# Kernel tuning notes

Measured on AMD Instinct MI355X. Metric: run time of the kernel, lower is better.

## Reference

```python
import jax, jax.numpy as jnp
import numpy as np

N, IN_DIM, HID, B, C = 131072, 256, 256, 8, 128


def setup_inputs() -> dict:
    key = jax.random.key(0)
    ks = jax.random.split(key, 7)
    s_in, s_h = 1.0 / np.sqrt(IN_DIM), 1.0 / np.sqrt(HID)
    return {
        "x": jax.random.normal(ks[0], (N, IN_DIM), dtype=jnp.float32),
        "W_base": jax.random.normal(ks[1], (IN_DIM, HID), dtype=jnp.float32) * s_in,
        "b_base": jax.random.normal(ks[2], (HID,), dtype=jnp.float32) * 0.01,
        "W_clf": jax.random.normal(ks[3], (B, HID, C), dtype=jnp.float32) * s_h,
        "b_clf": jax.random.normal(ks[4], (B, C), dtype=jnp.float32) * 0.01,
        "W_est": jax.random.normal(ks[5], (B, HID), dtype=jnp.float32) * s_h,
        "b_est": jax.random.normal(ks[6], (B,), dtype=jnp.float32) * 0.01,
    }


def reference(x, W_base, b_base, W_clf, b_clf, W_est, b_est):
    # base trunk: [N, HID]
    base_out = x @ W_base + b_base
    # per-branch estimated loss: [N, B]  (each branch's estimate_loss -> (N,1), viewed as (N,))
    est = base_out @ W_est.T + b_est
    # top-1 routing: per-sample argmin over branches (detached in original)
    branch_ids = jnp.argmin(est, axis=1)  # [N] int
    # all-branch logits [N, B, C]; selecting row branch_ids[n] reproduces the
    # per-branch gather -> forward -> scatter of the original exactly
    logits = jnp.einsum("nh,bhc->nbc", base_out, W_clf) + b_clf
    out = jnp.take_along_axis(logits, branch_ids[:, None, None], axis=1)[:, 0, :]  # [N, C]
    return out
```

## Files before the change

### kernel.cpp

```cpp
#include <hip/hip_runtime.h>


#define NROWS 131072

typedef __bf16 bf16x8 __attribute__((ext_vector_type(8)));
typedef float  f32x4  __attribute__((ext_vector_type(4)));
typedef unsigned short u16x8 __attribute__((ext_vector_type(8)));

__device__ __forceinline__ unsigned short f2bf(float f) {
    unsigned u = __builtin_bit_cast(unsigned, f);
    u += 0x7fffu + ((u >> 16) & 1u);
    return (unsigned short)(u >> 16);
}

__global__ __launch_bounds__(256) void k_prep(const float* __restrict__ Wb,
                                              const float* __restrict__ bb,
                                              const float* __restrict__ Wc,
                                              const float* __restrict__ bc,
                                              const float* __restrict__ We,
                                              const float* __restrict__ be,
                                              double* __restrict__ Wcomb,
                                              double* __restrict__ bcomb,
                                              unsigned short* __restrict__ Wfold,
                                              float* __restrict__ bfold,
                                              int* __restrict__ gzero) {
    __shared__ float clf[32][128];
    __shared__ float wbt[32][16];
    __shared__ double red[256];
    int blk = blockIdx.x, tid = threadIdx.x;

    if (blk < 8) {
        if (blk == 0 && tid < 16) gzero[tid] = 0;
        int b = blk, k = tid;
        const float4* wbr = (const float4*)(Wb + k * 256);
        const float4* wer = (const float4*)(We + b * 256);
        double a0 = 0.0, a1 = 0.0, a2 = 0.0, a3 = 0.0;
#pragma unroll 8
        for (int j = 0; j < 64; ++j) {
            float4 u = wbr[j], w = wer[j];
            a0 += (double)u.x * (double)w.x;
            a1 += (double)u.y * (double)w.y;
            a2 += (double)u.z * (double)w.z;
            a3 += (double)u.w * (double)w.w;
        }
        Wcomb[b * 256 + k] = (a0 + a1) + (a2 + a3);

        red[k] = (double)bb[k] * (double)We[b * 256 + k];
        __syncthreads();
        for (int s = 128; s; s >>= 1) {
            if (k < s) red[k] += red[k + s];
            __syncthreads();
        }
        if (k == 0) bcomb[b] = red[0] + (double)be[b];
        return;
    }

    if (blk < 12) {
        int b = (blk - 8) * 2 + (tid >> 7);
        int c = tid & 127;
        float a = bc[b * 128 + c];
        for (int h = 0; h < 256; ++h)
            a += bb[h] * Wc[(b * 256 + h) * 128 + c];
        bfold[b * 128 + c] = a;
        return;
    }

    int idx0 = blk - 12;
    int kg = idx0 & 15, b = idx0 >> 4;
    int c = tid & 127, kh = tid >> 7;

    float acc[8];
#pragma unroll
    for (int j = 0; j < 8; ++j) acc[j] = 0.f;

    for (int ht = 0; ht < 8; ++ht) {
#pragma unroll
        for (int j = 0; j < 16; ++j) {
            int idx = tid + j * 256;
            int hh = idx >> 7, cc = idx & 127;
            clf[hh][cc] = Wc[(b * 256 + ht * 32 + hh) * 128 + cc];
        }
#pragma unroll
        for (int j = 0; j < 2; ++j) {
            int idx = tid + j * 256;
            int hh = idx & 31, kk = idx >> 5;
            wbt[hh][kk] = Wb[(kg * 16 + kk) * 256 + ht * 32 + hh];
        }
        __syncthreads();
        for (int h = 0; h < 32; ++h) {
            float wc = clf[h][c];
            float4 w0 = *(const float4*)&wbt[h][kh * 8];
            float4 w1 = *(const float4*)&wbt[h][kh * 8 + 4];
            acc[0] += w0.x * wc; acc[1] += w0.y * wc;
            acc[2] += w0.z * wc; acc[3] += w0.w * wc;
            acc[4] += w1.x * wc; acc[5] += w1.y * wc;
            acc[6] += w1.z * wc; acc[7] += w1.w * wc;
        }
        __syncthreads();
    }
    unsigned short o8[8];
#pragma unroll
    for (int j = 0; j < 8; ++j) o8[j] = f2bf(acc[j]);
    u16x8 pk;
#pragma unroll
    for (int j = 0; j < 8; ++j) pk[j] = o8[j];
    int base = (b * 128 + c) * 256 + kg * 16 + kh * 8;
    *(u16x8*)&Wfold[base] = pk;
}

__global__ __launch_bounds__(256) void k_route1(const float* __restrict__ x,
                                                const double* __restrict__ Wcomb,
                                                const double* __restrict__ bcomb,
                                                unsigned char* __restrict__ bidg,
                                                int* __restrict__ gcnt) {
    __shared__ double wc[8 * 258];
    __shared__ double bco[8];
    __shared__ int cnt[8];
    __shared__ unsigned char bidl[32];
    int tid = threadIdx.x;

    for (int j = tid; j < 2048; j += 256) {
        int b = j >> 8, k = j & 255;
        wc[b * 258 + k] = Wcomb[j];
    }
    if (tid < 8) { bco[tid] = bcomb[tid]; cnt[tid] = 0; }
    __syncthreads();

    int b = tid & 7, oct = tid >> 3;
    int row = blockIdx.x * 32 + oct;
    const float* xr = x + (size_t)row * 256;
    const double* wcr = wc + b * 258;
    double a0 = bco[b], a1 = 0.0, a2 = 0.0, a3 = 0.0;
    for (int k = 0; k < 256; k += 8) {
        float4 xv0 = *(const float4*)(xr + k);
        float4 xv1 = *(const float4*)(xr + k + 4);
        double2 w0 = *(const double2*)(wcr + k);
        double2 w1 = *(const double2*)(wcr + k + 2);
        double2 w2 = *(const double2*)(wcr + k + 4);
        double2 w3 = *(const double2*)(wcr + k + 6);
        a0 += (double)xv0.x * w0.x; a1 += (double)xv0.y * w0.y;
        a2 += (double)xv0.z * w1.x; a3 += (double)xv0.w * w1.y;
        a0 += (double)xv1.x * w2.x; a1 += (double)xv1.y * w2.y;
        a2 += (double)xv1.z * w3.x; a3 += (double)xv1.w * w3.y;
    }
    double best = (a0 + a2) + (a1 + a3);
    int bbx = b;
    for (int d = 4; d; d >>= 1) {
        double o  = __shfl_down(best, (unsigned)d, 8);
        int    ob = __shfl_down(bbx,  (unsigned)d, 8);
        if (o < best || (o == best && ob < bbx)) { best = o; bbx = ob; }
    }
    if (b == 0) { bidl[oct] = (unsigned char)bbx; atomicAdd(&cnt[bbx], 1); }
    __syncthreads();
    if (tid < 32) bidg[blockIdx.x * 32 + tid] = bidl[tid];
    if (tid < 8 && cnt[tid]) atomicAdd(&gcnt[tid], cnt[tid]);
}

__global__ __launch_bounds__(256) void k_route2(const unsigned char* __restrict__ bidg,
                                                const int* __restrict__ gcnt,
                                                int* __restrict__ gofs,
                                                int* __restrict__ perm) {
    __shared__ int cnt[8], base8[8], gb[8];
    __shared__ unsigned short list[8][256];
    int tid = threadIdx.x;
    if (tid < 8) cnt[tid] = 0;
    __syncthreads();
    int row = blockIdx.x * 256 + tid;
    int b = bidg[row];
    int p = atomicAdd(&cnt[b], 1);
    list[b][p] = (unsigned short)tid;
    __syncthreads();
    if (tid == 0) {
        int s = 0;
        for (int i = 0; i < 8; ++i) { gb[i] = s; s += gcnt[i]; }
    }
    if (tid < 8) base8[tid] = cnt[tid] ? atomicAdd(&gofs[tid], cnt[tid]) : 0;
    __syncthreads();
    for (int j = tid; j < 2048; j += 256) {
        int bb2 = j >> 8, i = j & 255;
        if (i < cnt[bb2])
            perm[gb[bb2] + base8[bb2] + i] = blockIdx.x * 256 + (int)list[bb2][i];
    }
}

__global__ __launch_bounds__(256) void k_gemm(const float* __restrict__ x,
                                              const int* __restrict__ gcnt,
                                              const int* __restrict__ perm,
                                              const unsigned short* __restrict__ Wfold,
                                              const float* __restrict__ bfold,
                                              float* __restrict__ out) {
    __shared__ unsigned short xbf[64 * 264];
    __shared__ int rowid[64];
    int tid = threadIdx.x;

    int t = blockIdx.x;
    int b = -1, tile = 0, pb = 0, m = 0;
    int accT = 0, accR = 0;
#pragma unroll
    for (int i = 0; i < 8; ++i) {
        int ci = gcnt[i];
        int Ti = (ci + 63) >> 6;
        if (b < 0 && t < accT + Ti) {
            b = i; tile = t - accT; pb = accR;
            int rem = ci - tile * 64;
            m = rem < 64 ? rem : 64;
        }
        accT += Ti; accR += ci;
    }
    if (b < 0) return;

    int pbase = pb + tile * 64;
    if (tid < 64) rowid[tid] = perm[pbase + (tid < m ? tid : 0)];
    __syncthreads();

#pragma unroll 4
    for (int it = 0; it < 16; ++it) {
        int idx = it * 256 + tid;
        int r = idx >> 6, kq = idx & 63;
        float4 v = *(const float4*)(x + (size_t)rowid[r] * 256 + kq * 4);
        ushort4 pk4;
        pk4.x = f2bf(v.x); pk4.y = f2bf(v.y); pk4.z = f2bf(v.z); pk4.w = f2bf(v.w);
        *(ushort4*)&xbf[r * 264 + kq * 4] = pk4;
    }
    __syncthreads();

    int wave = tid >> 6, lane = tid & 63;
    int quad = lane >> 4, n16 = lane & 15;

    for (int cc = 0; cc < 2; ++cc) {
        int ct = wave + cc * 4;
        const unsigned short* wp = Wfold + ((size_t)(b * 128 + ct * 16 + n16)) * 256 + quad * 8;
        bf16x8 Bf[8];
#pragma unroll
        for (int kt = 0; kt < 8; ++kt)
            Bf[kt] = __builtin_bit_cast(bf16x8, *(const u16x8*)(wp + kt * 32));
        float bias = bfold[b * 128 + ct * 16 + n16];

        for (int rg = 0; rg < 4; ++rg) {
            int s = rg * 16;
            const unsigned short* ap = &xbf[(s + n16) * 264 + quad * 8];
            bf16x8 Af[8];
#pragma unroll
            for (int kt = 0; kt < 8; ++kt)
                Af[kt] = __builtin_bit_cast(bf16x8, *(const u16x8*)(ap + kt * 32));

            f32x4 acc = {bias, bias, bias, bias};
#pragma unroll
            for (int kt = 0; kt < 8; ++kt)
                acc = __builtin_amdgcn_mfma_f32_16x16x32_bf16(Af[kt], Bf[kt], acc, 0, 0, 0);

#pragma unroll
            for (int reg = 0; reg < 4; ++reg) {
                int r16 = s + quad * 4 + reg;
                if (r16 < m)
                    out[(size_t)rowid[r16] * 128 + ct * 16 + n16] = acc[reg];
            }
        }
    }
}

extern "C" void kernel_launch(void* const* d_in, const int* in_sizes, int n_in,
                              void* d_out, int out_size, void* d_ws, size_t ws_size,
                              hipStream_t stream) {
    const float* x  = (const float*)d_in[0];
    const float* Wb = (const float*)d_in[1];
    const float* bb = (const float*)d_in[2];
    const float* Wc = (const float*)d_in[3];
    const float* bc = (const float*)d_in[4];
    const float* We = (const float*)d_in[5];
    const float* be = (const float*)d_in[6];
    float* out = (float*)d_out;

    unsigned char* ws = (unsigned char*)d_ws;
    double* Wcomb = (double*)ws;
    double* bcomb = (double*)(ws + 16384);
    unsigned short* Wfold = (unsigned short*)(ws + 16448);
    float* bfold = (float*)(ws + 540736);
    int* gcnt = (int*)(ws + 544832);
    int* gofs = (int*)(ws + 544864);
    unsigned char* bidg = (unsigned char*)(ws + 544896);
    int* perm = (int*)(ws + 675968);

    hipLaunchKernelGGL(k_prep, dim3(140), dim3(256), 0, stream,
                       Wb, bb, Wc, bc, We, be, Wcomb, bcomb, Wfold, bfold, gcnt);
    hipLaunchKernelGGL(k_route1, dim3(NROWS / 32), dim3(256), 0, stream,
                       x, Wcomb, bcomb, bidg, gcnt);
    hipLaunchKernelGGL(k_route2, dim3(NROWS / 256), dim3(256), 0, stream,
                       bidg, gcnt, gofs, perm);
    hipLaunchKernelGGL(k_gemm, dim3(NROWS / 64 + 7), dim3(256), 0, stream,
                       x, gcnt, perm, Wfold, bfold, out);
}
```

Before: 299.4 us.

## Fuse routing, permutation and grouped GEMM into one per-tile kernel

Replaces the three-kernel route/permute/gemm pipeline with a single kernel. Each block loads 64 rows of x into LDS once, computes the fp64 routing scores from register-held combined weights, and buckets rows per branch locally. It then runs MFMA over 16-row groups per branch, reading Wfold straight from global/L2. This removes the second full read of x, the perm/bid global round trips, the global atomics and two launches. The cost is partially filled 16-row MFMA groups per branch in each block (up to 8 wasted groups), a large LDS footprint that limits occupancy, and every block re-reading branch weights. The bias-fold prep is also split across more blocks with a shared-memory reduction.

```diff
diff --git a/kernel.cpp b/kernel.cpp
--- a/kernel.cpp
+++ b/kernel.cpp
@@ -2,6 +2,8 @@
 
 
 #define NROWS 131072
+#define ROWS  64
+#define XST   260
 
 typedef __bf16 bf16x8 __attribute__((ext_vector_type(8)));
 typedef float  f32x4  __attribute__((ext_vector_type(4)));
@@ -22,15 +24,14 @@
                                               double* __restrict__ Wcomb,
                                               double* __restrict__ bcomb,
                                               unsigned short* __restrict__ Wfold,
-                                              float* __restrict__ bfold,
-                                              int* __restrict__ gzero) {
+                                              float* __restrict__ bfold) {
     __shared__ float clf[32][128];
     __shared__ float wbt[32][16];
     __shared__ double red[256];
+    __shared__ float part[256];
     int blk = blockIdx.x, tid = threadIdx.x;
 
     if (blk < 8) {
-        if (blk == 0 && tid < 16) gzero[tid] = 0;
         int b = blk, k = tid;
         const float4* wbr = (const float4*)(Wb + k * 256);
         const float4* wer = (const float4*)(We + b * 256);
@@ -55,17 +56,20 @@
         return;
     }
 
-    if (blk < 12) {
-        int b = (blk - 8) * 2 + (tid >> 7);
-        int c = tid & 127;
-        float a = bc[b * 128 + c];
-        for (int h = 0; h < 256; ++h)
-            a += bb[h] * Wc[(b * 256 + h) * 128 + c];
-        bfold[b * 128 + c] = a;
+    if (blk < 16) {
+        int b = blk - 8;
+        int c = tid & 127, hg = tid >> 7;
+        float a = 0.f;
+#pragma unroll 16
+        for (int h = 0; h < 128; ++h)
+            a += bb[hg * 128 + h] * Wc[((b * 256 + hg * 128 + h)) * 128 + c];
+        part[tid] = a;
+        __syncthreads();
+        if (tid < 128) bfold[b * 128 + tid] = part[tid] + part[tid + 128] + bc[b * 128 + tid];
         return;
     }
 
-    int idx0 = blk - 12;
+    int idx0 = blk - 16;
     int kg = idx0 & 15, b = idx0 >> 4;
     int c = tid & 127, kh = tid >> 7;
 
@@ -108,153 +112,138 @@
     *(u16x8*)&Wfold[base] = pk;
 }
 
-__global__ __launch_bounds__(256) void k_route1(const float* __restrict__ x,
-                                                const double* __restrict__ Wcomb,
-                                                const double* __restrict__ bcomb,
-                                                unsigned char* __restrict__ bidg,
-                                                int* __restrict__ gcnt) {
-    __shared__ double wc[8 * 258];
-    __shared__ double bco[8];
+__global__ __launch_bounds__(256, 2) void k_main(const float* __restrict__ x,
+                                                 const double* __restrict__ Wcomb,
+                                                 const double* __restrict__ bcomb,
+                                                 const unsigned short* __restrict__ Wfold,
+                                                 const float* __restrict__ bfold,
+                                                 float* __restrict__ out) {
+    __shared__ float xs[ROWS * XST];
+    __shared__ unsigned char list[8][ROWS];
     __shared__ int cnt[8];
-    __shared__ unsigned char bidl[32];
-    int tid = threadIdx.x;
-
-    for (int j = tid; j < 2048; j += 256) {
-        int b = j >> 8, k = j & 255;
-        wc[b * 258 + k] = Wcomb[j];
-    }
-    if (tid < 8) { bco[tid] = bcomb[tid]; cnt[tid] = 0; }
-    __syncthreads();
-
-    int b = tid & 7, oct = tid >> 3;
-    int row = blockIdx.x * 32 + oct;
-    const float* xr = x + (size_t)row * 256;
-    const double* wcr = wc + b * 258;
-    double a0 = bco[b], a1 = 0.0, a2 = 0.0, a3 = 0.0;
-    for (int k = 0; k < 256; k += 8) {
-        float4 xv0 = *(const float4*)(xr + k);
-        float4 xv1 = *(const float4*)(xr + k + 4);
-        double2 w0 = *(const double2*)(wcr + k);
-        double2 w1 = *(const double2*)(wcr + k + 2);
-        double2 w2 = *(const double2*)(wcr + k + 4);
-        double2 w3 = *(const double2*)(wcr + k + 6);
-        a0 += (double)xv0.x * w0.x; a1 += (double)xv0.y * w0.y;
-        a2 += (double)xv0.z * w1.x; a3 += (double)xv0.w * w1.y;
-        a0 += (double)xv1.x * w2.x; a1 += (double)xv1.y * w2.y;
-        a2 += (double)xv1.z * w3.x; a3 += (double)xv1.w * w3.y;
-    }
-    double best = (a0 + a2) + (a1 + a3);
-    int bbx = b;
-    for (int d = 4; d; d >>= 1) {
-        double o  = __shfl_down(best, (unsigned)d, 8);
-        int    ob = __shfl_down(bbx,  (unsigned)d, 8);
-        if (o < best || (o == best && ob < bbx)) { best = o; bbx = ob; }
-    }
-    if (b == 0) { bidl[oct] = (unsigned char)bbx; atomicAdd(&cnt[bbx], 1); }
-    __syncthreads();
-    if (tid < 32) bidg[blockIdx.x * 32 + tid] = bidl[tid];
-    if (tid < 8 && cnt[tid]) atomicAdd(&gcnt[tid], cnt[tid]);
-}
-
-__global__ __launch_bounds__(256) void k_route2(const unsigned char* __restrict__ bidg,
-                                                const int* __restrict__ gcnt,
-                                                int* __restrict__ gofs,
-                                                int* __restrict__ perm) {
-    __shared__ int cnt[8], base8[8], gb[8];
-    __shared__ unsigned short list[8][256];
-    int tid = threadIdx.x;
+    __shared__ unsigned char tasks[16];
+    __shared__ int ntasks;
+
+    const int tid = threadIdx.x;
+    const int blk = blockIdx.x;
+    const int wave = tid >> 6, lane = tid & 63;
+    const int bl = lane & 7, kc = lane >> 3;
+    const size_t rowbase = (size_t)blk * ROWS;
+
     if (tid < 8) cnt[tid] = 0;
-    __syncthreads();
-    int row = blockIdx.x * 256 + tid;
-    int b = bidg[row];
-    int p = atomicAdd(&cnt[b], 1);
-    list[b][p] = (unsigned short)tid;
-    __syncthreads();
-    if (tid == 0) {
-        int s = 0;
-        for (int i = 0; i < 8; ++i) { gb[i] = s; s += gcnt[i]; }
-    }
-    if (tid < 8) base8[tid] = cnt[tid] ? atomicAdd(&gofs[tid], cnt[tid]) : 0;
-    __syncthreads();
-    for (int j = tid; j < 2048; j += 256) {
-        int bb2 = j >> 8, i = j & 255;
-        if (i < cnt[bb2])
-            perm[gb[bb2] + base8[bb2] + i] = blockIdx.x * 256 + (int)list[bb2][i];
-    }
-}
-
-__global__ __launch_bounds__(256) void k_gemm(const float* __restrict__ x,
-                                              const int* __restrict__ gcnt,
-                                              const int* __restrict__ perm,
-                                              const unsigned short* __restrict__ Wfold,
-                                              const float* __restrict__ bfold,
-                                              float* __restrict__ out) {
-    __shared__ unsigned short xbf[64 * 264];
-    __shared__ int rowid[64];
-    int tid = threadIdx.x;
-
-    int t = blockIdx.x;
-    int b = -1, tile = 0, pb = 0, m = 0;
-    int accT = 0, accR = 0;
-#pragma unroll
-    for (int i = 0; i < 8; ++i) {
-        int ci = gcnt[i];
-        int Ti = (ci + 63) >> 6;
-        if (b < 0 && t < accT + Ti) {
-            b = i; tile = t - accT; pb = accR;
-            int rem = ci - tile * 64;
-            m = rem < 64 ? rem : 64;
-        }
-        accT += Ti; accR += ci;
-    }
-    if (b < 0) return;
-
-    int pbase = pb + tile * 64;
-    if (tid < 64) rowid[tid] = perm[pbase + (tid < m ? tid : 0)];
-    __syncthreads();
+
+    double w0[8], w1[8], w2[8], w3[8];
+    {
+        const double* wb = Wcomb + bl * 256 + kc * 4;
+#pragma unroll
+        for (int t = 0; t < 8; ++t) {
+            double2 p0 = *(const double2*)(wb + t * 32);
+            double2 p1 = *(const double2*)(wb + t * 32 + 2);
+            w0[t] = p0.x; w1[t] = p0.y; w2[t] = p1.x; w3[t] = p1.y;
+        }
+    }
+    const double bco = bcomb[bl];
 
 #pragma unroll 4
     for (int it = 0; it < 16; ++it) {
         int idx = it * 256 + tid;
-        int r = idx >> 6, kq = idx & 63;
-        float4 v = *(const float4*)(x + (size_t)rowid[r] * 256 + kq * 4);
-        ushort4 pk4;
-        pk4.x = f2bf(v.x); pk4.y = f2bf(v.y); pk4.z = f2bf(v.z); pk4.w = f2bf(v.w);
-        *(ushort4*)&xbf[r * 264 + kq * 4] = pk4;
+        int r = idx >> 6, gq = idx & 63;
+        float4 v = *(const float4*)(x + (rowbase + r) * 256 + gq * 4);
+        *(float4*)&xs[r * XST + gq * 4] = v;
     }
     __syncthreads();
 
-    int wave = tid >> 6, lane = tid & 63;
-    int quad = lane >> 4, n16 = lane & 15;
-
-    for (int cc = 0; cc < 2; ++cc) {
-        int ct = wave + cc * 4;
-        const unsigned short* wp = Wfold + ((size_t)(b * 128 + ct * 16 + n16)) * 256 + quad * 8;
-        bf16x8 Bf[8];
-#pragma unroll
-        for (int kt = 0; kt < 8; ++kt)
-            Bf[kt] = __builtin_bit_cast(bf16x8, *(const u16x8*)(wp + kt * 32));
-        float bias = bfold[b * 128 + ct * 16 + n16];
-
-        for (int rg = 0; rg < 4; ++rg) {
-            int s = rg * 16;
-            const unsigned short* ap = &xbf[(s + n16) * 264 + quad * 8];
-            bf16x8 Af[8];
-#pragma unroll
-            for (int kt = 0; kt < 8; ++kt)
-                Af[kt] = __builtin_bit_cast(bf16x8, *(const u16x8*)(ap + kt * 32));
-
-            f32x4 acc = {bias, bias, bias, bias};
-#pragma unroll
-            for (int kt = 0; kt < 8; ++kt)
-                acc = __builtin_amdgcn_mfma_f32_16x16x32_bf16(Af[kt], Bf[kt], acc, 0, 0, 0);
-
-#pragma unroll
-            for (int reg = 0; reg < 4; ++reg) {
-                int r16 = s + quad * 4 + reg;
-                if (r16 < m)
-                    out[(size_t)rowid[r16] * 128 + ct * 16 + n16] = acc[reg];
+    for (int rr = 0; rr < 16; ++rr) {
+        int r = wave * 16 + rr;
+        const float* xr = xs + r * XST + kc * 4;
+        double a0 = 0.0, a1 = 0.0, a2 = 0.0, a3 = 0.0;
+#pragma unroll
+        for (int t = 0; t < 8; ++t) {
+            float4 v = *(const float4*)(xr + t * 32);
+            a0 += (double)v.x * w0[t];
+            a1 += (double)v.y * w1[t];
+            a2 += (double)v.z * w2[t];
+            a3 += (double)v.w * w3[t];
+        }
+        double e = (a0 + a2) + (a1 + a3);
+        e += __shfl_xor(e, 8);
+        e += __shfl_xor(e, 16);
+        e += __shfl_xor(e, 32);
+        e += bco;
+        int bid = bl;
+#pragma unroll
+        for (int d = 4; d; d >>= 1) {
+            double o = __shfl_xor(e, d);
+            int ob = __shfl_xor(bid, d);
+            if (o < e || (o == e && ob < bid)) { e = o; bid = ob; }
+        }
+        if (lane == 0) {
+            int p = atomicAdd(&cnt[bid], 1);
+            list[bid][p] = (unsigned char)r;
+        }
+    }
+    __syncthreads();
+
+    if (tid == 0) {
+        int nt = 0;
+#pragma unroll
+        for (int b = 0; b < 8; ++b) {
+            int ng = (cnt[b] + 15) >> 4;
+            for (int g = 0; g < ng; ++g) tasks[nt++] = (unsigned char)((b << 4) | g);
+        }
+        ntasks = nt;
+    }
+    __syncthreads();
+
+    const int n16 = lane & 15, quad = lane >> 4;
+    const int nt = ntasks;
+    for (int t = wave; t < nt; t += 4) {
+        int b = tasks[t] >> 4, g = tasks[t] & 15;
+        int nb = cnt[b];
+        int slot = g * 16 + n16;
+        int arid = list[b][slot < nb ? slot : nb - 1];
+        const float* ap = xs + arid * XST + quad * 8;
+
+        bf16x8 Af[8];
+#pragma unroll
+        for (int kt = 0; kt < 8; ++kt) {
+            float4 f0 = *(const float4*)(ap + kt * 32);
+            float4 f1 = *(const float4*)(ap + kt * 32 + 4);
+            u16x8 pk;
+            pk[0] = f2bf(f0.x); pk[1] = f2bf(f0.y); pk[2] = f2bf(f0.z); pk[3] = f2bf(f0.w);
+            pk[4] = f2bf(f1.x); pk[5] = f2bf(f1.y); pk[6] = f2bf(f1.z); pk[7] = f2bf(f1.w);
+            Af[kt] = __builtin_bit_cast(bf16x8, pk);
+        }
+
+        const unsigned short* wb = Wfold + (size_t)(b * 128 + n16) * 256 + quad * 8;
+        f32x4 acc[8];
+#pragma unroll
+        for (int ct = 0; ct < 8; ++ct) {
+            float bias = bfold[b * 128 + ct * 16 + n16];
+            acc[ct] = (f32x4){bias, bias, bias, bias};
+        }
+#pragma unroll
+        for (int kt = 0; kt < 8; ++kt) {
+            const unsigned short* wk = wb + kt * 32;
+#pragma unroll
+            for (int ct = 0; ct < 8; ++ct) {
+                bf16x8 Bf = __builtin_bit_cast(bf16x8, *(const u16x8*)(wk + ct * 16 * 256));
+                acc[ct] = __builtin_amdgcn_mfma_f32_16x16x32_bf16(Af[kt], Bf, acc[ct], 0, 0, 0);
             }
+        }
+
+        int srow[4];
+#pragma unroll
+        for (int reg = 0; reg < 4; ++reg) {
+            int r16 = g * 16 + quad * 4 + reg;
+            srow[reg] = r16 < nb ? (int)list[b][r16] : -1;
+        }
+#pragma unroll
+        for (int ct = 0; ct < 8; ++ct) {
+#pragma unroll
+            for (int reg = 0; reg < 4; ++reg)
+                if (srow[reg] >= 0)
+                    out[(rowbase + srow[reg]) * 128 + ct * 16 + n16] = acc[ct][reg];
         }
     }
 }
@@ -276,17 +265,9 @@
     double* bcomb = (double*)(ws + 16384);
     unsigned short* Wfold = (unsigned short*)(ws + 16448);
     float* bfold = (float*)(ws + 540736);
-    int* gcnt = (int*)(ws + 544832);
-    int* gofs = (int*)(ws + 544864);
-    unsigned char* bidg = (unsigned char*)(ws + 544896);
-    int* perm = (int*)(ws + 675968);
-
-    hipLaunchKernelGGL(k_prep, dim3(140), dim3(256), 0, stream,
-                       Wb, bb, Wc, bc, We, be, Wcomb, bcomb, Wfold, bfold, gcnt);
-    hipLaunchKernelGGL(k_route1, dim3(NROWS / 32), dim3(256), 0, stream,
-                       x, Wcomb, bcomb, bidg, gcnt);
-    hipLaunchKernelGGL(k_route2, dim3(NROWS / 256), dim3(256), 0, stream,
-                       bidg, gcnt, gofs, perm);
-    hipLaunchKernelGGL(k_gemm, dim3(NROWS / 64 + 7), dim3(256), 0, stream,
-                       x, gcnt, perm, Wfold, bfold, out);
-}
+
+    hipLaunchKernelGGL(k_prep, dim3(144), dim3(256), 0, stream,
+                       Wb, bb, Wc, bc, We, be, Wcomb, bcomb, Wfold, bfold);
+    hipLaunchKernelGGL(k_main, dim3(NROWS / ROWS), dim3(256), 0, stream,
+                       x, Wcomb, bcomb, Wfold, bfold, out);
+}
```

Result: slower. 369.9 us (+23.5%).
